# Performance work log

Hardware: AMD Instinct MI355X
Metric: run time of the kernel (lower is better)

Reference implementation:

```python
import jax, jax.numpy as jnp
import numpy as np

COMMA_ID = 1010  # ',' in bert-base-uncased vocab
N_HEADS = 8
BN_EPS = 1e-5


def setup_inputs() -> dict:
    key = jax.random.key(0)
    ks = jax.random.split(key, 12)
    B, S, D = 64, 512, 768
    sc = 0.02
    text_hs = jax.random.normal(ks[0], (B, S, D), jnp.float32)
    cols_hs = jax.random.normal(ks[1], (B, S, D), jnp.float32)
    # column input ids: random non-comma tokens, commas planted every 16 positions -> 32 commas/row, 33 segments
    col_ids = jax.random.randint(ks[2], (B, S), 2000, 30000, dtype=jnp.int32)
    col_ids = col_ids.at[:, ::16].set(COMMA_ID)
    Wq = jax.random.normal(ks[3], (D, D), jnp.float32) * sc
    Wk = jax.random.normal(ks[4], (D, D), jnp.float32) * sc
    Wv = jax.random.normal(ks[5], (D, D), jnp.float32) * sc
    Wo = jax.random.normal(ks[6], (D, D), jnp.float32) * sc
    bq = jnp.zeros((D,), jnp.float32)
    bk = jnp.zeros((D,), jnp.float32)
    bv = jnp.zeros((D,), jnp.float32)
    bo = jnp.zeros((D,), jnp.float32)
    gamma = jnp.ones((S,), jnp.float32)
    beta = jnp.zeros((S,), jnp.float32)
    w_out = jax.random.normal(ks[7], (D, 1), jnp.float32) * sc
    b_out = jnp.zeros((1,), jnp.float32)
    return {"text_hs": text_hs, "cols_hs": cols_hs, "col_ids": col_ids, "n_segments": 33,
            "Wq": Wq, "bq": bq, "Wk": Wk, "bk": bk, "Wv": Wv, "bv": bv, "Wo": Wo, "bo": bo,
            "gamma": gamma, "beta": beta, "w_out": w_out, "b_out": b_out}


def reference(text_hs, cols_hs, col_ids, n_segments,
              Wq, bq, Wk, bk, Wv, bv, Wo, bo, gamma, beta, w_out, b_out):
    B, S, D = text_hs.shape
    hd = D // N_HEADS
    # cross attention: query = columns, key/value = text (torch MultiheadAttention, batch_first)
    q = (cols_hs @ Wq.T + bq).reshape(B, S, N_HEADS, hd)
    k = (text_hs @ Wk.T + bk).reshape(B, S, N_HEADS, hd)
    v = (text_hs @ Wv.T + bv).reshape(B, S, N_HEADS, hd)
    scores = jnp.einsum('bqhd,bkhd->bhqk', q, k) / jnp.sqrt(jnp.asarray(hd, q.dtype))
    attn = jax.nn.softmax(scores, axis=-1)
    o = jnp.einsum('bhqk,bkhd->bqhd', attn, v).reshape(B, S, D)
    attn_out = o @ Wo.T + bo  # [B,S,D]
    # BatchNorm1d(S) in training mode: per-seq-position channel stats over (batch, D)
    mean = attn_out.mean(axis=(0, 2), keepdims=True)
    var = jnp.mean((attn_out - mean) ** 2, axis=(0, 2), keepdims=True)
    bn = (attn_out - mean) / jnp.sqrt(var + BN_EPS) * gamma[None, :, None] + beta[None, :, None]
    # residual add + scalar head -> per-token score [B,S]
    ret = ((cols_hs + bn) @ w_out + b_out)[..., 0]
    # compose_outputs: segment-sum over comma-delimited spans, comma tokens excluded
    is_comma = col_ids == COMMA_ID
    seg = jnp.cumsum(is_comma.astype(jnp.int32), axis=1)  # commas before each non-comma token
    vals = jnp.where(is_comma, jnp.zeros((), ret.dtype), ret)
    flat_seg = (jnp.arange(B, dtype=jnp.int32)[:, None] * n_segments + seg).reshape(-1)
    out = jax.ops.segment_sum(vals.reshape(-1), flat_seg, num_segments=B * n_segments)
    return out.reshape(B, n_segments)
```

## Files before the change

kernel.cpp:

```cpp
#include <hip/hip_runtime.h>
#include <hip/hip_bf16.h>
#include <math.h>

typedef __attribute__((ext_vector_type(8))) short bf16x8;
typedef __attribute__((ext_vector_type(4))) float f32x4;

#define COMMA_ID 1010
#define S 512
#define D 768
#define NH 8
#define HD 96

__device__ __forceinline__ ushort f2bf(float f) {
  union { float f; unsigned u; } v; v.f = f;
  unsigned u = v.u;
  return (ushort)((u + 0x7fffu + ((u >> 16) & 1u)) >> 16);
}
__device__ __forceinline__ float bf2f(ushort h) {
  union { unsigned u; float f; } v; v.u = ((unsigned)h) << 16; return v.f;
}

__device__ __forceinline__ void async16(void* lds, const void* g) {
  __builtin_amdgcn_global_load_lds(
      (const __attribute__((address_space(1))) unsigned int*)g,
      (__attribute__((address_space(3))) unsigned int*)lds, 16, 0, 0);
}

__device__ __forceinline__ f32x4 mfma16(bf16x8 a, bf16x8 b, f32x4 c) {
  return __builtin_amdgcn_mfma_f32_16x16x32_bf16(a, b, c, 0, 0, 0);
}

__global__ __launch_bounds__(256) void cvt2_kernel(const float* __restrict__ a, ushort* __restrict__ oa,
                                                   const float* __restrict__ b, ushort* __restrict__ ob_,
                                                   int n8each) {
  int i = blockIdx.x * 256 + threadIdx.x;
  const float* in; ushort* out; int j;
  if (i < n8each) { in = a; out = oa; j = i; }
  else { in = b; out = ob_; j = i - n8each; if (j >= n8each) return; }
  const float4* p = ((const float4*)in) + (size_t)j * 2;
  float4 x = p[0], y = p[1];
  bf16x8 o;
  o[0] = (short)f2bf(x.x); o[1] = (short)f2bf(x.y); o[2] = (short)f2bf(x.z); o[3] = (short)f2bf(x.w);
  o[4] = (short)f2bf(y.x); o[5] = (short)f2bf(y.y); o[6] = (short)f2bf(y.z); o[7] = (short)f2bf(y.w);
  ((bf16x8*)out)[j] = o;
}

__global__ __launch_bounds__(256) void cvtW_kernel(
    const float* __restrict__ w0, const float* __restrict__ w1,
    const float* __restrict__ w2, const float* __restrict__ w3,
    ushort* __restrict__ o0, ushort* __restrict__ o1,
    ushort* __restrict__ o2, ushort* __restrict__ o3,
    int n8, float sc0) {
  int i = blockIdx.x * 256 + threadIdx.x;
  int sel = i / n8, j = i - sel * n8;
  if (sel >= 4) return;
  const float* in = sel == 0 ? w0 : sel == 1 ? w1 : sel == 2 ? w2 : w3;
  ushort* out = sel == 0 ? o0 : sel == 1 ? o1 : sel == 2 ? o2 : o3;
  float sc = sel == 0 ? sc0 : 1.0f;
  const float4* p = ((const float4*)in) + (size_t)j * 2;
  float4 x = p[0], y = p[1];
  bf16x8 o;
  o[0] = (short)f2bf(x.x * sc); o[1] = (short)f2bf(x.y * sc); o[2] = (short)f2bf(x.z * sc); o[3] = (short)f2bf(x.w * sc);
  o[4] = (short)f2bf(y.x * sc); o[5] = (short)f2bf(y.y * sc); o[6] = (short)f2bf(y.z * sc); o[7] = (short)f2bf(y.w * sc);
  ((bf16x8*)out)[j] = o;
}

#define BM 128
#define BN 128
#define BK 64
#define KDIM 768
#define NDIM 768

template<int MODE>
__global__ __launch_bounds__(256, 3) void gemm_bf16(
    const ushort* __restrict__ A0, const ushort* __restrict__ A1,
    const ushort* __restrict__ W0, const ushort* __restrict__ W1,
    const float* __restrict__ bias0, const float* __restrict__ bias1,
    const float* __restrict__ bias2, float bscale0,
    ushort* __restrict__ C0, ushort* __restrict__ C1, ushort* __restrict__ C2,
    const float* __restrict__ wv, float* __restrict__ sum_s,
    float* __restrict__ sq_s, float* __restrict__ c2,
    int qblocks, int NT0, int NT1)
{
  int nwg = gridDim.x, cpx = nwg >> 3;
  int l = (blockIdx.x & 7) * cpx + (blockIdx.x >> 3);
  int seg1 = (l >= qblocks);
  int ls = seg1 ? l - qblocks : l;
  int NTILES = seg1 ? NT1 : NT0;
  const ushort* A = seg1 ? A1 : A0;
  const ushort* W = seg1 ? W1 : W0;
  float bscale = seg1 ? 1.0f : bscale0;
  int mt = ls / NTILES, nt = ls % NTILES;
  int m0 = mt * BM, n0 = nt * BN;
  int sel = (n0 >= NDIM);
  int cbase = n0 - (sel ? NDIM : 0);
  const float* bi = seg1 ? (sel ? bias2 : bias1) : bias0;
  ushort* Co = seg1 ? (sel ? C2 : C1) : C0;
  int tid = threadIdx.x;
  int w = tid >> 6, lane = tid & 63;
  int wr = w >> 1, wc = w & 1;
  int lr = lane & 15, ks = lane >> 4;
  __shared__ __align__(16) ushort As[BM * BK];
  __shared__ __align__(16) ushort Bs[BN * BK];
  f32x4 acc[4][4] = {};
  const ushort* Arow = A + (size_t)m0 * KDIM;
  const ushort* Wrow = W + (size_t)n0 * KDIM;
  int srow = tid >> 3, sch = tid & 7;

  auto STAGE = [&](int k0) {
#pragma unroll
    for (int i = 0; i < 4; ++i) {
      int row = i * 32 + srow;
      int scc = sch ^ (row & 7);
      async16(&As[(row * 8 + sch) * 8], Arow + (size_t)row * KDIM + k0 + scc * 8);
      async16(&Bs[(row * 8 + sch) * 8], Wrow + (size_t)row * KDIM + k0 + scc * 8);
    }
  };
  auto COMPUTE = [&]() {
    bf16x8 a[4][2], b[4][2];
#pragma unroll
    for (int m = 0; m < 4; m++) {
      int row = wr * 64 + m * 16 + lr;
#pragma unroll
      for (int kk = 0; kk < 2; kk++) {
        int cc = kk * 4 + ks;
        a[m][kk] = *(const bf16x8*)&As[(row * 8 + (cc ^ (row & 7))) * 8];
      }
    }
#pragma unroll
    for (int n = 0; n < 4; n++) {
      int row = wc * 64 + n * 16 + lr;
#pragma unroll
      for (int kk = 0; kk < 2; kk++) {
        int cc = kk * 4 + ks;
        b[n][kk] = *(const bf16x8*)&Bs[(row * 8 + (cc ^ (row & 7))) * 8];
      }
    }
#pragma unroll
    for (int m = 0; m < 4; m++)
#pragma unroll
      for (int n = 0; n < 4; n++) {
        acc[m][n] = mfma16(a[m][0], b[n][0], acc[m][n]);
        acc[m][n] = mfma16(a[m][1], b[n][1], acc[m][n]);
      }
  };

  for (int k0 = 0; k0 < KDIM; k0 += BK) {
    STAGE(k0);
    __syncthreads();
    COMPUTE();
    __syncthreads();
  }

  float bnv[4];
#pragma unroll
  for (int n = 0; n < 4; n++) bnv[n] = bi[cbase + wc * 64 + n * 16 + lr] * bscale;

  if (MODE == 0) {
#pragma unroll
    for (int m = 0; m < 4; m++) {
      int grow = m0 + wr * 64 + m * 16 + ks * 4;
#pragma unroll
      for (int r = 0; r < 4; r++) {
        ushort* cp = Co + (size_t)(grow + r) * NDIM + cbase + wc * 64 + lr;
#pragma unroll
        for (int n = 0; n < 4; n++) cp[n * 16] = f2bf(acc[m][n][r] + bnv[n]);
      }
    }
  } else {
    float wn[4];
#pragma unroll
    for (int n = 0; n < 4; n++) wn[n] = wv[cbase + wc * 64 + n * 16 + lr];
#pragma unroll
    for (int m = 0; m < 4; m++) {
#pragma unroll
      for (int r = 0; r < 4; r++) {
        float ps = 0.f, pq = 0.f, pw = 0.f;
#pragma unroll
        for (int n = 0; n < 4; n++) {
          float v = acc[m][n][r] + bnv[n];
          ps += v; pq += v * v; pw += v * wn[n];
        }
#pragma unroll
        for (int mk = 1; mk < 16; mk <<= 1) {
          ps += __shfl_xor(ps, mk);
          pq += __shfl_xor(pq, mk);
          pw += __shfl_xor(pw, mk);
        }
        if (lr == 0) {
          int grow = m0 + wr * 64 + m * 16 + ks * 4 + r;
          atomicAdd(&sum_s[grow & (S - 1)], ps);
          atomicAdd(&sq_s[grow & (S - 1)], pq);
          atomicAdd(&c2[grow], pw);
        }
      }
    }
  }
}

__global__ __launch_bounds__(256) void transpose_v(const ushort* __restrict__ vb,
                                                   ushort* __restrict__ vt) {
  int blk = blockIdx.x;
  int dt = blk % 3; int st = (blk / 3) % (S / 32); int h = (blk / (3 * (S / 32))) % NH;
  int b = blk / (3 * (S / 32) * NH);
  __shared__ ushort t[32][33];
  int i = threadIdx.x >> 5, j = threadIdx.x & 31;
  int s0 = st * 32, d0 = dt * 32;
#pragma unroll
  for (int k = 0; k < 4; k++) {
    int s = s0 + i + k * 8;
    t[i + k * 8][j] = vb[((size_t)(b * S + s)) * D + h * HD + d0 + j];
  }
  __syncthreads();
#pragma unroll
  for (int k = 0; k < 4; k++) {
    int d = d0 + i + k * 8;
    vt[((size_t)((b * NH + h) * HD + d)) * S + s0 + j] = t[j][i + k * 8];
  }
}

__global__ __launch_bounds__(256, 3) void attn_kernel(const ushort* __restrict__ qb,
                                                      const ushort* __restrict__ kb,
                                                      const ushort* __restrict__ vt,
                                                      ushort* __restrict__ ob) {
  int wgid = blockIdx.x;
  int xcd = wgid & 7, t1 = wgid >> 3;
  int qt = t1 & 3, phi = t1 >> 2;
  int p = phi * 8 + xcd;
  int b = p >> 3, h = p & 7;
  int tid = threadIdx.x;
  int w = tid >> 6, lane = tid & 63;
  int lr = lane & 15, ks = lane >> 4;
  int q0 = qt * 128 + w * 32;

  __shared__ __align__(16) ushort Ks[6144];
  __shared__ __align__(16) ushort Vs[2][6144];
  __shared__ __align__(16) ushort Pb[4][1152];
  ushort* Pw = &Pb[w][0];

  const size_t bS = (size_t)b * S;
  const ushort* qptr = qb + (bS + q0 + lr) * D + h * HD;
  bf16x8 aq[2][3];
#pragma unroll
  for (int m = 0; m < 2; m++)
#pragma unroll
    for (int x = 0; x < 3; x++)
      aq[m][x] = *(const bf16x8*)(qptr + (size_t)m * 16 * D + x * 32 + ks * 8);

  float l_part[2][4] = {};
  f32x4 oacc[2][6] = {};

  const ushort* kbase = kb + bS * D + h * HD;
  const ushort* vbase = vt + (size_t)((b * NH + h) * HD) * S;

  auto STAGE_K = [&](int kv0) {
#pragma unroll
    for (int i = 0; i < 3; i++) {
      int c = w + 4 * i;
      async16(&Ks[(c * 64 + lane) * 8], kbase + (size_t)(kv0 + lane) * D + c * 8);
    }
  };
  auto STAGE_V = [&](int buf, int kv0) {
#pragma unroll
    for (int i = 0; i < 3; i++) {
      int u = (w + 4 * i) * 64 + lane;
      int cc = u / 96, d = u - cc * 96;
      async16(&Vs[buf][(size_t)u * 8], vbase + (size_t)d * S + kv0 + cc * 8);
    }
  };

  STAGE_K(0);
  STAGE_V(0, 0);
  __syncthreads();

  for (int it = 0; it < 8; ++it) {
    int cur = it & 1;
    f32x4 st[2][4];
#pragma unroll
    for (int t = 0; t < 4; t++) {
      bf16x8 bk[3];
#pragma unroll
      for (int x = 0; x < 3; x++)
        bk[x] = *(const bf16x8*)&Ks[((x * 4 + ks) * 64 + t * 16 + lr) * 8];
#pragma unroll
      for (int m = 0; m < 2; m++) {
        f32x4 s = {};
        s = mfma16(aq[m][0], bk[0], s);
        s = mfma16(aq[m][1], bk[1], s);
        s = mfma16(aq[m][2], bk[2], s);
        st[m][t] = s;
      }
    }
    __syncthreads();
    if (it < 7) { STAGE_K((it + 1) * 64); STAGE_V(cur ^ 1, (it + 1) * 64); }
    bf16x8 pa[2][2];
#pragma unroll
    for (int m = 0; m < 2; m++) {
#pragma unroll
      for (int t = 0; t < 4; t++)
#pragma unroll
        for (int r = 0; r < 4; r++) {
          float e = exp2f(st[m][t][r]);
          l_part[m][r] += e;
          Pw[(ks * 4 + r) * 72 + t * 16 + lr] = f2bf(e);
        }
#pragma unroll
      for (int kk = 0; kk < 2; kk++)
        pa[m][kk] = *(const bf16x8*)&Pw[lr * 72 + kk * 32 + ks * 8];
    }
    const ushort* Vb = &Vs[cur][0];
#pragma unroll
    for (int kk = 0; kk < 2; kk++)
#pragma unroll
      for (int n = 0; n < 6; n++) {
        bf16x8 bv = *(const bf16x8*)&Vb[((kk * 4 + ks) * 96 + n * 16 + lr) * 8];
        oacc[0][n] = mfma16(pa[0][kk], bv, oacc[0][n]);
        oacc[1][n] = mfma16(pa[1][kk], bv, oacc[1][n]);
      }
    __syncthreads();
  }

  float inv[2][4];
#pragma unroll
  for (int m = 0; m < 2; m++)
#pragma unroll
    for (int r = 0; r < 4; r++) {
      float s = l_part[m][r];
#pragma unroll
      for (int mk = 1; mk < 16; mk <<= 1) s += __shfl_xor(s, mk);
      inv[m][r] = 1.0f / s;
    }
  ushort* optr = ob + (bS + q0) * D + h * HD;
#pragma unroll
  for (int m = 0; m < 2; m++)
#pragma unroll
    for (int n = 0; n < 6; n++)
#pragma unroll
      for (int r = 0; r < 4; r++)
        optr[(size_t)(m * 16 + ks * 4 + r) * D + n * 16 + lr] = f2bf(oacc[m][n][r] * inv[m][r]);
}

__global__ __launch_bounds__(256) void c1_dot(const ushort* __restrict__ colsb,
                                              const float* __restrict__ wv,
                                              float* __restrict__ c1) {
  int row = blockIdx.x * 4 + (threadIdx.x >> 6);
  int lane = threadIdx.x & 63;
  const ushort* rp = colsb + (size_t)row * D;
  float s = 0.f;
  bf16x8 a = *(const bf16x8*)(rp + lane * 8);
#pragma unroll
  for (int j = 0; j < 8; j++) s += bf2f((ushort)a[j]) * wv[lane * 8 + j];
  ushort4 b4 = *(const ushort4*)(rp + 512 + lane * 4);
  s += bf2f(b4.x) * wv[512 + lane * 4 + 0];
  s += bf2f(b4.y) * wv[512 + lane * 4 + 1];
  s += bf2f(b4.z) * wv[512 + lane * 4 + 2];
  s += bf2f(b4.w) * wv[512 + lane * 4 + 3];
#pragma unroll
  for (int mk = 1; mk < 64; mk <<= 1) s += __shfl_xor(s, mk);
  if (lane == 0) c1[row] = s;
}

__global__ __launch_bounds__(512) void finalize_kernel(
    const float* __restrict__ sum_s, const float* __restrict__ sq_s,
    const float* __restrict__ c1, const float* __restrict__ c2,
    const float* __restrict__ gamma, const float* __restrict__ beta,
    const float* __restrict__ wv, const float* __restrict__ b_out,
    const int* __restrict__ ids, float* __restrict__ out, int nseg, float invBD)
{
  int b = blockIdx.x, s = threadIdx.x;
  int wid = s >> 6, lane = s & 63;
  __shared__ float wpart[8];
  __shared__ int wtot[8];
  __shared__ float seg_acc[64];
  float wval = wv[s] + (s < (D - S) ? wv[S + s] : 0.f);
  float t = wval;
#pragma unroll
  for (int mk = 1; mk < 64; mk <<= 1) t += __shfl_xor(t, mk);
  if (lane == 0) wpart[wid] = t;
  int row = b * S + s;
  bool comma = (ids[row] == COMMA_ID);
  unsigned long long mask = __ballot(comma);
  if (lane == 0) wtot[wid] = __popcll(mask);
  if (s < 64) seg_acc[s] = 0.f;
  __syncthreads();
  float Sw = 0.f;
#pragma unroll
  for (int i = 0; i < 8; i++) Sw += wpart[i];
  float mean = sum_s[s] * invBD;
  float var = sq_s[s] * invBD - mean * mean;
  float alpha = gamma[s] * rsqrtf(var + 1e-5f);
  float shift = beta[s] - mean * alpha;
  float ret = c1[row] + b_out[0] + alpha * c2[row] + shift * Sw;
  int base = 0;
  for (int i = 0; i < wid; i++) base += wtot[i];
  int seg = base + __popcll(mask & ((1ull << lane) - 1ull)) + (comma ? 1 : 0);
  if (!comma && seg < nseg) atomicAdd(&seg_acc[seg], ret);
  __syncthreads();
  if (s < nseg) out[b * nseg + s] = seg_acc[s];
}

extern "C" void kernel_launch(void* const* d_in, const int* in_sizes, int n_in,
                              void* d_out, int out_size, void* d_ws, size_t ws_size,
                              hipStream_t stream) {
  const float* text = (const float*)d_in[0];
  const float* cols = (const float*)d_in[1];
  const int* ids = (const int*)d_in[2];
  const float* Wq = (const float*)d_in[4];
  const float* bq = (const float*)d_in[5];
  const float* Wk = (const float*)d_in[6];
  const float* bk = (const float*)d_in[7];
  const float* Wv = (const float*)d_in[8];
  const float* bv = (const float*)d_in[9];
  const float* Wo = (const float*)d_in[10];
  const float* bo = (const float*)d_in[11];
  const float* gamma = (const float*)d_in[12];
  const float* beta = (const float*)d_in[13];
  const float* wv = (const float*)d_in[14];
  const float* b_out = (const float*)d_in[15];

  const int B = in_sizes[0] / (S * D);
  const int M = B * S;
  const int nseg = out_size / B;
  const size_t NE = (size_t)B * S * D;
  const size_t big = NE * 2;
  const float qscale = 0.10206207262f * 1.44269504089f;

  char* ws = (char*)d_ws;
  size_t off = 0;
  auto alloc = [&](size_t bytes) { void* p = ws + off; off = (off + bytes + 255) & ~(size_t)255; return p; };
  ushort* ws0 = (ushort*)alloc(big);
  ushort* ws1 = (ushort*)alloc(big);
  ushort* qb  = (ushort*)alloc(big);
  ushort* kb  = (ushort*)alloc(big);
  ushort* Wq_b = (ushort*)alloc((size_t)D * D * 2);
  ushort* Wk_b = (ushort*)alloc((size_t)D * D * 2);
  ushort* Wv_b = (ushort*)alloc((size_t)D * D * 2);
  ushort* Wo_b = (ushort*)alloc((size_t)D * D * 2);
  float* sum_s = (float*)alloc(S * 4);
  float* sq_s  = (float*)alloc(S * 4);
  float* c1    = (float*)alloc((size_t)M * 4);
  float* c2    = (float*)alloc((size_t)M * 4);
  bool merged = (off + big) <= ws_size;
  ushort* vbig = merged ? (ushort*)alloc(big) : nullptr;

  ushort* text_b = ws0; ushort* cols_b = ws1;
  ushort* vb = merged ? vbig : ws1;
  ushort* vt = ws0;
  ushort* ob = ws1;

  int n8 = (int)(NE / 8);
  cvt2_kernel<<<(2 * n8 + 255) / 256, 256, 0, stream>>>(text, text_b, cols, cols_b, n8);
  int w8 = D * D / 8;
  cvtW_kernel<<<(4 * w8 + 255) / 256, 256, 0, stream>>>(Wq, Wk, Wv, Wo, Wq_b, Wk_b, Wv_b, Wo_b, w8, qscale);

  hipMemsetAsync(sum_s, 0, S * 4, stream);
  hipMemsetAsync(sq_s, 0, S * 4, stream);
  hipMemsetAsync(c2, 0, (size_t)M * 4, stream);

  c1_dot<<<M / 4, 256, 0, stream>>>(cols_b, wv, c1);

  int qblocks = (M / BM) * 6;
  if (merged) {
    int gall = qblocks + (M / BM) * 12;
    gemm_bf16<0><<<gall, 256, 0, stream>>>(cols_b, text_b, Wq_b, Wk_b,
                                           bq, bk, bv, qscale,
                                           qb, kb, vb,
                                           nullptr, nullptr, nullptr, nullptr,
                                           qblocks, 6, 12);
  } else {
    gemm_bf16<0><<<qblocks, 256, 0, stream>>>(cols_b, cols_b, Wq_b, Wq_b,
                                              bq, bq, bq, qscale,
                                              qb, qb, qb,
                                              nullptr, nullptr, nullptr, nullptr,
                                              qblocks, 6, 6);
    int g12 = (M / BM) * 12;
    gemm_bf16<0><<<g12, 256, 0, stream>>>(text_b, text_b, Wk_b, Wk_b,
                                          bk, bk, bv, 1.0f,
                                          kb, kb, vb,
                                          nullptr, nullptr, nullptr, nullptr,
                                          0, 12, 12);
  }

  transpose_v<<<B * NH * (S / 32) * 3, 256, 0, stream>>>(vb, vt);

  attn_kernel<<<B * NH * 4, 256, 0, stream>>>(qb, kb, vt, ob);

  gemm_bf16<1><<<qblocks, 256, 0, stream>>>(ob, ob, Wo_b, Wo_b,
                                            bo, bo, bo, 1.0f,
                                            nullptr, nullptr, nullptr,
                                            wv, sum_s, sq_s, c2,
                                            qblocks, 6, 6);

  finalize_kernel<<<B, 512, 0, stream>>>(sum_s, sq_s, c1, c2, gamma, beta, wv, b_out, ids,
                                         (float*)d_out, nseg, 1.0f / (float)(B * D));
}
```

Measured before the change: 400.7 us.

## Fuse V transpose into QKV GEMM epilogue and narrow output-projection tiles

The merged QKV GEMM now writes V directly in head-transposed [b,h,d,s] layout from its epilogue, which removes the separate transpose_v kernel and its full read/write pass over V. The GEMM is templated on N-tile width, and the output-projection GEMM uses 64-wide N tiles, doubling its grid to fill more CUs. The transposed stores are 8-byte scattered writes, which may coalesce worse, and the narrower tiles reuse A less.

```diff
diff --git a/kernel.cpp b/kernel.cpp
--- a/kernel.cpp
+++ b/kernel.cpp
@@ -66,12 +66,11 @@
 }
 
 #define BM 128
-#define BN 128
 #define BK 64
 #define KDIM 768
 #define NDIM 768
 
-template<int MODE>
+template<int MODE, int BNT>
 __global__ __launch_bounds__(256, 3) void gemm_bf16(
     const ushort* __restrict__ A0, const ushort* __restrict__ A1,
     const ushort* __restrict__ W0, const ushort* __restrict__ W1,
@@ -80,8 +79,9 @@
     ushort* __restrict__ C0, ushort* __restrict__ C1, ushort* __restrict__ C2,
     const float* __restrict__ wv, float* __restrict__ sum_s,
     float* __restrict__ sq_s, float* __restrict__ c2,
-    int qblocks, int NT0, int NT1)
+    int qblocks, int NT0, int NT1, int vtr)
 {
+  const int BN = BNT * 32;
   int nwg = gridDim.x, cpx = nwg >> 3;
   int l = (blockIdx.x & 7) * cpx + (blockIdx.x >> 3);
   int seg1 = (l >= qblocks);
@@ -101,8 +101,8 @@
   int wr = w >> 1, wc = w & 1;
   int lr = lane & 15, ks = lane >> 4;
   __shared__ __align__(16) ushort As[BM * BK];
-  __shared__ __align__(16) ushort Bs[BN * BK];
-  f32x4 acc[4][4] = {};
+  __shared__ __align__(16) ushort Bs[BNT * 32 * BK];
+  f32x4 acc[4][BNT] = {};
   const ushort* Arow = A + (size_t)m0 * KDIM;
   const ushort* Wrow = W + (size_t)n0 * KDIM;
   int srow = tid >> 3, sch = tid & 7;
@@ -113,11 +113,16 @@
       int row = i * 32 + srow;
       int scc = sch ^ (row & 7);
       async16(&As[(row * 8 + sch) * 8], Arow + (size_t)row * KDIM + k0 + scc * 8);
+    }
+#pragma unroll
+    for (int i = 0; i < BNT; ++i) {
+      int row = i * 32 + srow;
+      int scc = sch ^ (row & 7);
       async16(&Bs[(row * 8 + sch) * 8], Wrow + (size_t)row * KDIM + k0 + scc * 8);
     }
   };
   auto COMPUTE = [&]() {
-    bf16x8 a[4][2], b[4][2];
+    bf16x8 a[4][2], b[BNT][2];
 #pragma unroll
     for (int m = 0; m < 4; m++) {
       int row = wr * 64 + m * 16 + lr;
@@ -128,8 +133,8 @@
       }
     }
 #pragma unroll
-    for (int n = 0; n < 4; n++) {
-      int row = wc * 64 + n * 16 + lr;
+    for (int n = 0; n < BNT; n++) {
+      int row = wc * (BNT * 16) + n * 16 + lr;
 #pragma unroll
       for (int kk = 0; kk < 2; kk++) {
         int cc = kk * 4 + ks;
@@ -139,7 +144,7 @@
 #pragma unroll
     for (int m = 0; m < 4; m++)
 #pragma unroll
-      for (int n = 0; n < 4; n++) {
+      for (int n = 0; n < BNT; n++) {
         acc[m][n] = mfma16(a[m][0], b[n][0], acc[m][n]);
         acc[m][n] = mfma16(a[m][1], b[n][1], acc[m][n]);
       }
@@ -152,32 +157,51 @@
     __syncthreads();
   }
 
-  float bnv[4];
-#pragma unroll
-  for (int n = 0; n < 4; n++) bnv[n] = bi[cbase + wc * 64 + n * 16 + lr] * bscale;
+  float bnv[BNT];
+#pragma unroll
+  for (int n = 0; n < BNT; n++) bnv[n] = bi[cbase + wc * (BNT * 16) + n * 16 + lr] * bscale;
 
   if (MODE == 0) {
-#pragma unroll
-    for (int m = 0; m < 4; m++) {
-      int grow = m0 + wr * 64 + m * 16 + ks * 4;
-#pragma unroll
-      for (int r = 0; r < 4; r++) {
-        ushort* cp = Co + (size_t)(grow + r) * NDIM + cbase + wc * 64 + lr;
-#pragma unroll
-        for (int n = 0; n < 4; n++) cp[n * 16] = f2bf(acc[m][n][r] + bnv[n]);
+    if (vtr && sel) {
+#pragma unroll
+      for (int m = 0; m < 4; m++) {
+        int grow = m0 + wr * 64 + m * 16 + ks * 4;
+        int b = grow >> 9, s0 = grow & (S - 1);
+#pragma unroll
+        for (int n = 0; n < BNT; n++) {
+          int col = cbase + wc * (BNT * 16) + n * 16 + lr;
+          int h = col / HD, d = col - h * HD;
+          ushort4 v4;
+          v4.x = f2bf(acc[m][n][0] + bnv[n]);
+          v4.y = f2bf(acc[m][n][1] + bnv[n]);
+          v4.z = f2bf(acc[m][n][2] + bnv[n]);
+          v4.w = f2bf(acc[m][n][3] + bnv[n]);
+          *(ushort4*)&Co[((size_t)((b * NH + h) * HD + d)) * S + s0] = v4;
+        }
+      }
+    } else {
+#pragma unroll
+      for (int m = 0; m < 4; m++) {
+        int grow = m0 + wr * 64 + m * 16 + ks * 4;
+#pragma unroll
+        for (int r = 0; r < 4; r++) {
+          ushort* cp = Co + (size_t)(grow + r) * NDIM + cbase + wc * (BNT * 16) + lr;
+#pragma unroll
+          for (int n = 0; n < BNT; n++) cp[n * 16] = f2bf(acc[m][n][r] + bnv[n]);
+        }
       }
     }
   } else {
-    float wn[4];
-#pragma unroll
-    for (int n = 0; n < 4; n++) wn[n] = wv[cbase + wc * 64 + n * 16 + lr];
+    float wn[BNT];
+#pragma unroll
+    for (int n = 0; n < BNT; n++) wn[n] = wv[cbase + wc * (BNT * 16) + n * 16 + lr];
 #pragma unroll
     for (int m = 0; m < 4; m++) {
 #pragma unroll
       for (int r = 0; r < 4; r++) {
         float ps = 0.f, pq = 0.f, pw = 0.f;
 #pragma unroll
-        for (int n = 0; n < 4; n++) {
+        for (int n = 0; n < BNT; n++) {
           float v = acc[m][n][r] + bnv[n];
           ps += v; pq += v * v; pw += v * wn[n];
         }
@@ -444,8 +468,7 @@
   ushort* vbig = merged ? (ushort*)alloc(big) : nullptr;
 
   ushort* text_b = ws0; ushort* cols_b = ws1;
-  ushort* vb = merged ? vbig : ws1;
-  ushort* vt = ws0;
+  ushort* vt = merged ? vbig : ws0;
   ushort* ob = ws1;
 
   int n8 = (int)(NE / 8);
@@ -462,34 +485,34 @@
   int qblocks = (M / BM) * 6;
   if (merged) {
     int gall = qblocks + (M / BM) * 12;
-    gemm_bf16<0><<<gall, 256, 0, stream>>>(cols_b, text_b, Wq_b, Wk_b,
-                                           bq, bk, bv, qscale,
-                                           qb, kb, vb,
-                                           nullptr, nullptr, nullptr, nullptr,
-                                           qblocks, 6, 12);
+    gemm_bf16<0, 4><<<gall, 256, 0, stream>>>(cols_b, text_b, Wq_b, Wk_b,
+                                              bq, bk, bv, qscale,
+                                              qb, kb, vbig,
+                                              nullptr, nullptr, nullptr, nullptr,
+                                              qblocks, 6, 12, 1);
   } else {
-    gemm_bf16<0><<<qblocks, 256, 0, stream>>>(cols_b, cols_b, Wq_b, Wq_b,
-                                              bq, bq, bq, qscale,
-                                              qb, qb, qb,
-                                              nullptr, nullptr, nullptr, nullptr,
-                                              qblocks, 6, 6);
+    gemm_bf16<0, 4><<<qblocks, 256, 0, stream>>>(cols_b, cols_b, Wq_b, Wq_b,
+                                                 bq, bq, bq, qscale,
+                                                 qb, qb, qb,
+                                                 nullptr, nullptr, nullptr, nullptr,
+                                                 qblocks, 6, 6, 0);
     int g12 = (M / BM) * 12;
-    gemm_bf16<0><<<g12, 256, 0, stream>>>(text_b, text_b, Wk_b, Wk_b,
-                                          bk, bk, bv, 1.0f,
-                                          kb, kb, vb,
-                                          nullptr, nullptr, nullptr, nullptr,
-                                          0, 12, 12);
+    gemm_bf16<0, 4><<<g12, 256, 0, stream>>>(text_b, text_b, Wk_b, Wk_b,
+                                             bk, bk, bv, 1.0f,
+                                             kb, kb, ws1,
+                                             nullptr, nullptr, nullptr, nullptr,
+                                             0, 12, 12, 0);
+    transpose_v<<<B * NH * (S / 32) * 3, 256, 0, stream>>>(ws1, ws0);
   }
 
-  transpose_v<<<B * NH * (S / 32) * 3, 256, 0, stream>>>(vb, vt);
-
   attn_kernel<<<B * NH * 4, 256, 0, stream>>>(qb, kb, vt, ob);
 
-  gemm_bf16<1><<<qblocks, 256, 0, stream>>>(ob, ob, Wo_b, Wo_b,
-                                            bo, bo, bo, 1.0f,
-                                            nullptr, nullptr, nullptr,
-                                            wv, sum_s, sq_s, c2,
-                                            qblocks, 6, 6);
+  int og = (M / BM) * 12;
+  gemm_bf16<1, 2><<<og, 256, 0, stream>>>(ob, ob, Wo_b, Wo_b,
+                                          bo, bo, bo, 1.0f,
+                                          nullptr, nullptr, nullptr,
+                                          wv, sum_s, sq_s, c2,
+                                          og + 1, 12, 12, 0);
 
   finalize_kernel<<<B, 512, 0, stream>>>(sum_s, sq_s, c1, c2, gamma, beta, wv, b_out, ids,
                                          (float*)d_out, nseg, 1.0f / (float)(B * D));
```

Result: slower. 481.6 us (+20.2%).
